# Kernel optimization log

Measured on AMD Instinct MI355X. Metric: run time of the kernel, lower is better.

Reference implementation:

```python
import jax, jax.numpy as jnp
import numpy as np

HIDDEN = 1024
HEADS = 16
BATCH = 2
SEQ = 2048
# dropout_p = 0.1 but module evaluated in eval mode (training=False) -> identity


def setup_inputs() -> dict:
    key = jax.random.key(0)
    k1, k2, k3 = jax.random.split(key, 3)
    x = jax.random.normal(k1, (BATCH, SEQ, HIDDEN), dtype=jnp.float32)
    # unit-scaling Linear: weight ~ N(0,1) (reset_parameters uses nn.init.normal_)
    w_qkv = jax.random.normal(k2, (3 * HIDDEN, HIDDEN), dtype=jnp.float32)
    w_o = jax.random.normal(k3, (HIDDEN, HIDDEN), dtype=jnp.float32)
    return {"x": x, "w_qkv": w_qkv, "w_o": w_o}


def reference(x, w_qkv, w_o):
    b, s, hid = x.shape
    heads = HEADS
    d = hid // heads
    # unit-scaled linear (constraint='to_output_scale'): y = x @ W.T * fan_in**-0.5
    qkv = (x @ w_qkv.T) * (hid ** -0.5)            # [b, s, 3*hid]
    # einops 'b s (z h d) -> z b h s d'
    qkv = qkv.reshape(b, s, 3, heads, d)
    q = jnp.transpose(qkv[:, :, 0], (0, 2, 1, 3))   # [b, h, s, d]
    k = jnp.transpose(qkv[:, :, 1], (0, 2, 1, 3))
    v = jnp.transpose(qkv[:, :, 2], (0, 2, 1, 3))
    # unit-scaled matmul: scale = inner_dim**-0.5
    scores = jnp.einsum('bhqd,bhkd->bhqk', q, k) * (d ** -0.5)  # [b, h, s, s]
    # unit-scaled softmax: output_scale = n / sqrt(n - 1)
    attn = jax.nn.softmax(scores, axis=-1) * (s / np.sqrt(s - 1.0))
    # dropout inactive (eval mode)
    out = jnp.einsum('bhqk,bhkd->bhqd', attn, v) * (s ** -0.5)  # inner dim = s
    out = jnp.transpose(out, (0, 2, 1, 3)).reshape(b, s, hid)   # 'b h s d -> b s (h d)'
    return (out @ w_o.T) * (hid ** -0.5)
```

## Files before the change

kernel.cpp:

```cpp
#include <hip/hip_runtime.h>

typedef unsigned short u16;
typedef _Float16 f16x8 __attribute__((ext_vector_type(8)));
typedef float f32x4 __attribute__((ext_vector_type(4)));
typedef unsigned short u16x4 __attribute__((ext_vector_type(4)));

#define HID 1024
#define SEQ 2048
#define NH 16
#define DH 64

__device__ __forceinline__ u16 f2h(float f) {
  return __builtin_bit_cast(u16, (_Float16)f);
}
__device__ __forceinline__ f32x4 mfma_h(f16x8 a, f16x8 b, f32x4 c) {
  return __builtin_amdgcn_mfma_f32_16x16x32_f16(a, b, c, 0, 0, 0);
}
__device__ __forceinline__ float fexp2(float x) {
#if __has_builtin(__builtin_amdgcn_exp2f)
  return __builtin_amdgcn_exp2f(x);
#else
  return __expf(0.69314718f * x);
#endif
}
__device__ __forceinline__ void g2l16(const u16* g, u16* l) {
  __builtin_amdgcn_global_load_lds(
      (const __attribute__((address_space(1))) unsigned int*)g,
      (__attribute__((address_space(3))) unsigned int*)l, 16, 0, 0);
}

#define NX4 ((4096 * 1024) / 4)
#define NQ4 ((3072 * 1024) / 4)
#define NO4 ((1024 * 1024) / 4)
__global__ __launch_bounds__(256) void prep_kernel(
    const float* __restrict__ x, const float* __restrict__ wq,
    const float* __restrict__ wo,
    u16* __restrict__ x16, u16* __restrict__ wq16,
    u16* __restrict__ wo_h, u16* __restrict__ wo_l) {
  int i = blockIdx.x * 256 + threadIdx.x;
  if (i < NX4) {
    const float4 v = ((const float4*)x)[i];
    u16x4 o;
    o[0] = f2h(v.x); o[1] = f2h(v.y); o[2] = f2h(v.z); o[3] = f2h(v.w);
    *(u16x4*)&x16[i * 4] = o;
  } else if (i < NX4 + NQ4) {
    int k = i - NX4;
    const float4 v = ((const float4*)wq)[k];
    u16x4 o;
    o[0] = f2h(v.x); o[1] = f2h(v.y); o[2] = f2h(v.z); o[3] = f2h(v.w);
    *(u16x4*)&wq16[k * 4] = o;
  } else {
    int k = i - NX4 - NQ4;
    const float4 v = ((const float4*)wo)[k];
    float vv[4] = {v.x, v.y, v.z, v.w};
    u16x4 h, l;
#pragma unroll
    for (int j = 0; j < 4; ++j) {
      _Float16 hh = (_Float16)vv[j];
      h[j] = __builtin_bit_cast(u16, hh);
      l[j] = f2h(vv[j] - (float)hh);
    }
    *(u16x4*)&wo_h[k * 4] = h;
    *(u16x4*)&wo_l[k * 4] = l;
  }
}

__global__ __launch_bounds__(256, 3) void gemm_qkv(
    const u16* __restrict__ a16, const u16* __restrict__ b16,
    u16* __restrict__ qf, u16* __restrict__ kf, u16* __restrict__ vtf) {
  __shared__ __align__(16) u16 la[128 * 32], lb[128 * 32];
  const int t = threadIdx.x;
  const int lane = t & 63, w = t >> 6;
  const int wr = w >> 1, wc = w & 1;
  const int lr = lane & 15, lg = lane >> 4;
  const int br = blockIdx.x, bc = blockIdx.y;
  const f32x4 fzero = {0.f, 0.f, 0.f, 0.f};
  f32x4 acc[4][4];
#pragma unroll
  for (int i = 0; i < 4; ++i)
#pragma unroll
    for (int j = 0; j < 4; ++j) acc[i][j] = fzero;
  const int srow = t >> 2, scol = (t & 3) << 3;
  const u16* ga = a16 + (size_t)(br * 128 + srow) * HID + scol;
  const u16* gb = b16 + (size_t)(bc * 128 + srow) * HID + scol;
  const int lo16 = t * 8;
  for (int kk = 0; kk < HID; kk += 32) {
    g2l16(ga + kk, &la[lo16]);
    g2l16(ga + kk + (size_t)64 * HID, &la[lo16 + 2048]);
    g2l16(gb + kk, &lb[lo16]);
    g2l16(gb + kk + (size_t)64 * HID, &lb[lo16 + 2048]);
    __syncthreads();
    f16x8 ah[4], bh[4];
#pragma unroll
    for (int i = 0; i < 4; ++i)
      ah[i] = *(const f16x8*)&la[(wr * 64 + i * 16 + lr) * 32 + lg * 8];
#pragma unroll
    for (int j = 0; j < 4; ++j)
      bh[j] = *(const f16x8*)&lb[(wc * 64 + j * 16 + lr) * 32 + lg * 8];
#pragma unroll
    for (int i = 0; i < 4; ++i)
#pragma unroll
      for (int j = 0; j < 4; ++j) acc[i][j] = mfma_h(ah[i], bh[j], acc[i][j]);
    __syncthreads();
  }
  const int m0 = br * 128 + wr * 64, n0 = bc * 128 + wc * 64;
#pragma unroll
  for (int i = 0; i < 4; ++i)
#pragma unroll
    for (int j = 0; j < 4; ++j)
#pragma unroll
      for (int r = 0; r < 4; ++r) {
        int row = m0 + i * 16 + lg * 4 + r;
        int col = n0 + j * 16 + lr;
        float val = acc[i][j][r] * 0.03125f;
        int b = row >> 11, s = row & 2047;
        int z = col >> 10, hh = (col >> 6) & 15, d = col & 63;
        int bhid = b * NH + hh;
        if (z == 0) {
          qf[((size_t)bhid * SEQ + s) * DH + d] = f2h(val * 0.18033688f);
        } else if (z == 1) {
          kf[((size_t)bhid * SEQ + s) * DH + d] = f2h(val);
        } else {
          int s2 = (s & ~63) | ((s & 15) << 2) | ((s >> 4) & 3);
          vtf[((size_t)bhid * DH + d) * SEQ + s2] = f2h(val);
        }
      }
}

__global__ __launch_bounds__(256, 2) void gemm_proj(
    const u16* __restrict__ a16,
    const u16* __restrict__ b_hi, const u16* __restrict__ b_lo,
    float* __restrict__ out) {
  __shared__ __align__(16) u16 la[128 * 32];
  __shared__ __align__(16) u16 lbh[64 * 32], lbl[64 * 32];
  const int t = threadIdx.x;
  const int lane = t & 63, w = t >> 6;
  const int wr = w >> 1, wc = w & 1;
  const int lr = lane & 15, lg = lane >> 4;
  const int br = blockIdx.x, bc = blockIdx.y;
  const f32x4 fzero = {0.f, 0.f, 0.f, 0.f};
  f32x4 acc[4][2];
#pragma unroll
  for (int i = 0; i < 4; ++i)
#pragma unroll
    for (int j = 0; j < 2; ++j) acc[i][j] = fzero;
  const int srow = t >> 2, scol = (t & 3) << 3;
  const u16* ga = a16 + (size_t)(br * 128 + srow) * HID + scol;
  const u16* gbh = b_hi + (size_t)(bc * 64 + srow) * HID + scol;
  const u16* gbl = b_lo + (size_t)(bc * 64 + srow) * HID + scol;
  const int lo16 = t * 8;
  for (int kk = 0; kk < HID; kk += 32) {
    g2l16(ga + kk, &la[lo16]);
    g2l16(ga + kk + (size_t)64 * HID, &la[lo16 + 2048]);
    g2l16(gbh + kk, &lbh[lo16]);
    g2l16(gbl + kk, &lbl[lo16]);
    __syncthreads();
    f16x8 ah[4], bh[2], bl[2];
#pragma unroll
    for (int i = 0; i < 4; ++i)
      ah[i] = *(const f16x8*)&la[(wr * 64 + i * 16 + lr) * 32 + lg * 8];
#pragma unroll
    for (int j = 0; j < 2; ++j) {
      int o = (wc * 32 + j * 16 + lr) * 32 + lg * 8;
      bh[j] = *(const f16x8*)&lbh[o];
      bl[j] = *(const f16x8*)&lbl[o];
    }
#pragma unroll
    for (int i = 0; i < 4; ++i)
#pragma unroll
      for (int j = 0; j < 2; ++j) {
        acc[i][j] = mfma_h(ah[i], bh[j], acc[i][j]);
        acc[i][j] = mfma_h(ah[i], bl[j], acc[i][j]);
      }
    __syncthreads();
  }
  const int m0 = br * 128 + wr * 64, n0 = bc * 64 + wc * 32;
#pragma unroll
  for (int i = 0; i < 4; ++i)
#pragma unroll
    for (int j = 0; j < 2; ++j)
#pragma unroll
      for (int r = 0; r < 4; ++r) {
        int row = m0 + i * 16 + lg * 4 + r;
        int col = n0 + j * 16 + lr;
        out[(size_t)row * HID + col] = acc[i][j][r] * 0.03125f;
      }
}

__global__ __launch_bounds__(256, 2) void attn_kernel(
    const u16* __restrict__ qf, const u16* __restrict__ kf,
    const u16* __restrict__ vtf, u16* __restrict__ o16) {
  __shared__ __align__(16) u16 lk[2][64 * 64];
  __shared__ __align__(16) u16 lv[2][64 * 64];
  __shared__ __align__(16) u16 lp[128 * 64];
  const int t = threadIdx.x;
  const int lane = t & 63, w = t >> 6;
  const int lr = lane & 15, lg = lane >> 4;
  const int bh = blockIdx.x, qt = blockIdx.y;
  const size_t base_qk = (size_t)bh * SEQ * DH;
  const size_t base_vt = (size_t)bh * DH * SEQ;

  f16x8 qfr[2][2];
#pragma unroll
  for (int rt = 0; rt < 2; ++rt)
#pragma unroll
    for (int ks = 0; ks < 2; ++ks)
      qfr[rt][ks] = *(const f16x8*)&qf[base_qk +
          (size_t)(qt * 128 + w * 32 + rt * 16 + lr) * DH + ks * 32 + lg * 8];

  const f32x4 fzero = {0.f, 0.f, 0.f, 0.f};
  f32x4 acc_o[2][4];
  float l_i[2][4];
#pragma unroll
  for (int rt = 0; rt < 2; ++rt)
#pragma unroll
    for (int r = 0; r < 4; ++r) l_i[rt][r] = 0.f;
#pragma unroll
  for (int rt = 0; rt < 2; ++rt)
#pragma unroll
    for (int ct = 0; ct < 4; ++ct) acc_o[rt][ct] = fzero;

  const int srow = t >> 3;
  const int scol = ((t & 7) ^ (srow & 7)) << 3;
  const int lo16 = t * 8;

  const u16* gk0 = kf + base_qk + (size_t)srow * DH + scol;
  const u16* gv0 = vtf + base_vt + (size_t)srow * SEQ + scol;

#define STAGE(buf, j)                                             \
  {                                                               \
    const u16* gk = gk0 + (size_t)(j) * 64 * DH;                  \
    g2l16(gk, &lk[buf][lo16]);                                    \
    g2l16(gk + 32 * DH, &lk[buf][lo16 + 2048]);                   \
    const u16* gv = gv0 + (j) * 64;                               \
    g2l16(gv, &lv[buf][lo16]);                                    \
    g2l16(gv + (size_t)32 * SEQ, &lv[buf][lo16 + 2048]);          \
  }

  STAGE(0, 0)

  for (int j = 0; j < SEQ / 64; ++j) {
    const int cur = j & 1;
    __syncthreads();

    f32x4 sa[2][4];
#pragma unroll
    for (int rt = 0; rt < 2; ++rt)
#pragma unroll
      for (int ct = 0; ct < 4; ++ct) sa[rt][ct] = fzero;
#pragma unroll
    for (int ks = 0; ks < 2; ++ks)
#pragma unroll
      for (int ct = 0; ct < 4; ++ct) {
        int row = ct * 16 + lr;
        f16x8 kfr = *(const f16x8*)&lk[cur][row * 64 + (((ks * 4 + lg) ^ (row & 7)) << 3)];
#pragma unroll
        for (int rt = 0; rt < 2; ++rt) sa[rt][ct] = mfma_h(qfr[rt][ks], kfr, sa[rt][ct]);
      }

#pragma unroll
    for (int rt = 0; rt < 2; ++rt)
#pragma unroll
      for (int r = 0; r < 4; ++r) {
        float p0 = fexp2(sa[rt][0][r]);
        float p1 = fexp2(sa[rt][1][r]);
        float p2 = fexp2(sa[rt][2][r]);
        float p3 = fexp2(sa[rt][3][r]);
        l_i[rt][r] += (p0 + p1) + (p2 + p3);
        int prow = w * 32 + rt * 16 + lg * 4 + r;
        u16x4 pk;
        pk[0] = f2h(p0); pk[1] = f2h(p1); pk[2] = f2h(p2); pk[3] = f2h(p3);
        int phys = prow * 64 + ((((lr >> 1) ^ (prow & 7)) << 3) | ((lr & 1) << 2));
        *(u16x4*)&lp[phys] = pk;
      }
    __syncthreads();

    if (j + 1 < SEQ / 64) STAGE(cur ^ 1, j + 1)

#pragma unroll
    for (int ks = 0; ks < 2; ++ks) {
      f16x8 pfr[2];
#pragma unroll
      for (int rt = 0; rt < 2; ++rt) {
        int prow = w * 32 + rt * 16 + lr;
        pfr[rt] = *(const f16x8*)&lp[prow * 64 + (((ks * 4 + lg) ^ (prow & 7)) << 3)];
      }
#pragma unroll
      for (int ct = 0; ct < 4; ++ct) {
        int vrow = ct * 16 + lr;
        f16x8 vfr = *(const f16x8*)&lv[cur][vrow * 64 + (((ks * 4 + lg) ^ (vrow & 7)) << 3)];
#pragma unroll
        for (int rt = 0; rt < 2; ++rt) acc_o[rt][ct] = mfma_h(pfr[rt], vfr, acc_o[rt][ct]);
      }
    }
  }

#pragma unroll
  for (int rt = 0; rt < 2; ++rt)
#pragma unroll
    for (int r = 0; r < 4; ++r) {
      float l = l_i[rt][r];
      l += __shfl_xor(l, 1, 16);
      l += __shfl_xor(l, 2, 16);
      l += __shfl_xor(l, 4, 16);
      l += __shfl_xor(l, 8, 16);
      l_i[rt][r] = l;
    }

  const int b = bh >> 4, hh = bh & 15;
  const float fact = 1.00024426f;
#pragma unroll
  for (int rt = 0; rt < 2; ++rt)
#pragma unroll
    for (int r = 0; r < 4; ++r) {
      float inv = fact / l_i[rt][r];
      int s = qt * 128 + w * 32 + rt * 16 + lg * 4 + r;
#pragma unroll
      for (int ct = 0; ct < 4; ++ct) {
        int d = ct * 16 + lr;
        float val = acc_o[rt][ct][r] * inv;
        o16[((size_t)(b * SEQ + s)) * HID + hh * DH + d] = f2h(val);
      }
    }
}

extern "C" void kernel_launch(void* const* d_in, const int* in_sizes, int n_in,
                              void* d_out, int out_size, void* d_ws, size_t ws_size,
                              hipStream_t stream) {
  const float* x = (const float*)d_in[0];
  const float* w_qkv = (const float*)d_in[1];
  const float* w_o = (const float*)d_in[2];
  u16* ws = (u16*)d_ws;
  const size_t XS = (size_t)4096 * 1024;
  const size_t WQ = (size_t)3072 * 1024;
  const size_t WO = (size_t)1024 * 1024;
  u16* x16  = ws;           u16* wq16 = x16 + XS;
  u16* wo_h = wq16 + WQ;    u16* wo_l = wo_h + WO;
  u16* q_f  = wo_l + WO;    u16* k_f  = q_f + XS;
  u16* vt_f = k_f + XS;     u16* o16  = vt_f + XS;

  prep_kernel<<<(NX4 + NQ4 + NO4) / 256, 256, 0, stream>>>(
      x, w_qkv, w_o, x16, wq16, wo_h, wo_l);
  gemm_qkv<<<dim3(32, 24), 256, 0, stream>>>(x16, wq16, q_f, k_f, vt_f);
  attn_kernel<<<dim3(32, 16), 256, 0, stream>>>(q_f, k_f, vt_f, o16);
  gemm_proj<<<dim3(32, 16), 256, 0, stream>>>(o16, wo_h, wo_l, (float*)d_out);
}
```

Baseline: 189.8 us.

## Drop split-fp16 output weights, use 2-wave attention blocks, pack P conversion

Stops splitting the output-projection weight into hi/lo fp16 halves, which halves the MFMA count and B-tile traffic in gemm_proj at some cost in precision. The attention kernel now uses 128 threads per block, with each wave owning 64 query rows instead of 32. This doubles K/V fragment reuse per LDS read but raises register pressure and halves the waves available per block. The P tile is converted with packed cvt_pkrtz into a single 64-bit store, and the prep kernel is simplified to a single branchless conversion path.

```diff
diff --git a/kernel.cpp b/kernel.cpp
--- a/kernel.cpp
+++ b/kernel.cpp
@@ -23,6 +23,9 @@
   return __expf(0.69314718f * x);
 #endif
 }
+__device__ __forceinline__ unsigned pk2h(float a, float b) {
+  return __builtin_bit_cast(unsigned, __builtin_amdgcn_cvt_pkrtz(a, b));
+}
 __device__ __forceinline__ void g2l16(const u16* g, u16* l) {
   __builtin_amdgcn_global_load_lds(
       (const __attribute__((address_space(1))) unsigned int*)g,
@@ -35,34 +38,17 @@
 __global__ __launch_bounds__(256) void prep_kernel(
     const float* __restrict__ x, const float* __restrict__ wq,
     const float* __restrict__ wo,
-    u16* __restrict__ x16, u16* __restrict__ wq16,
-    u16* __restrict__ wo_h, u16* __restrict__ wo_l) {
+    u16* __restrict__ x16, u16* __restrict__ wq16, u16* __restrict__ wo16) {
   int i = blockIdx.x * 256 + threadIdx.x;
-  if (i < NX4) {
-    const float4 v = ((const float4*)x)[i];
-    u16x4 o;
-    o[0] = f2h(v.x); o[1] = f2h(v.y); o[2] = f2h(v.z); o[3] = f2h(v.w);
-    *(u16x4*)&x16[i * 4] = o;
-  } else if (i < NX4 + NQ4) {
-    int k = i - NX4;
-    const float4 v = ((const float4*)wq)[k];
-    u16x4 o;
-    o[0] = f2h(v.x); o[1] = f2h(v.y); o[2] = f2h(v.z); o[3] = f2h(v.w);
-    *(u16x4*)&wq16[k * 4] = o;
-  } else {
-    int k = i - NX4 - NQ4;
-    const float4 v = ((const float4*)wo)[k];
-    float vv[4] = {v.x, v.y, v.z, v.w};
-    u16x4 h, l;
-#pragma unroll
-    for (int j = 0; j < 4; ++j) {
-      _Float16 hh = (_Float16)vv[j];
-      h[j] = __builtin_bit_cast(u16, hh);
-      l[j] = f2h(vv[j] - (float)hh);
-    }
-    *(u16x4*)&wo_h[k * 4] = h;
-    *(u16x4*)&wo_l[k * 4] = l;
-  }
+  const float4 v = (i < NX4) ? ((const float4*)x)[i]
+                 : (i < NX4 + NQ4) ? ((const float4*)wq)[i - NX4]
+                 : ((const float4*)wo)[i - NX4 - NQ4];
+  u16* dst = (i < NX4) ? &x16[(size_t)i * 4]
+           : (i < NX4 + NQ4) ? &wq16[(size_t)(i - NX4) * 4]
+           : &wo16[(size_t)(i - NX4 - NQ4) * 4];
+  u16x4 o;
+  o[0] = f2h(v.x); o[1] = f2h(v.y); o[2] = f2h(v.z); o[3] = f2h(v.w);
+  *(u16x4*)dst = o;
 }
 
 __global__ __launch_bounds__(256, 3) void gemm_qkv(
@@ -128,11 +114,10 @@
 }
 
 __global__ __launch_bounds__(256, 2) void gemm_proj(
-    const u16* __restrict__ a16,
-    const u16* __restrict__ b_hi, const u16* __restrict__ b_lo,
+    const u16* __restrict__ a16, const u16* __restrict__ b16,
     float* __restrict__ out) {
   __shared__ __align__(16) u16 la[128 * 32];
-  __shared__ __align__(16) u16 lbh[64 * 32], lbl[64 * 32];
+  __shared__ __align__(16) u16 lb[64 * 32];
   const int t = threadIdx.x;
   const int lane = t & 63, w = t >> 6;
   const int wr = w >> 1, wc = w & 1;
@@ -146,32 +131,25 @@
     for (int j = 0; j < 2; ++j) acc[i][j] = fzero;
   const int srow = t >> 2, scol = (t & 3) << 3;
   const u16* ga = a16 + (size_t)(br * 128 + srow) * HID + scol;
-  const u16* gbh = b_hi + (size_t)(bc * 64 + srow) * HID + scol;
-  const u16* gbl = b_lo + (size_t)(bc * 64 + srow) * HID + scol;
+  const u16* gb = b16 + (size_t)(bc * 64 + srow) * HID + scol;
   const int lo16 = t * 8;
   for (int kk = 0; kk < HID; kk += 32) {
     g2l16(ga + kk, &la[lo16]);
     g2l16(ga + kk + (size_t)64 * HID, &la[lo16 + 2048]);
-    g2l16(gbh + kk, &lbh[lo16]);
-    g2l16(gbl + kk, &lbl[lo16]);
-    __syncthreads();
-    f16x8 ah[4], bh[2], bl[2];
+    g2l16(gb + kk, &lb[lo16]);
+    __syncthreads();
+    f16x8 ah[4], bh[2];
 #pragma unroll
     for (int i = 0; i < 4; ++i)
       ah[i] = *(const f16x8*)&la[(wr * 64 + i * 16 + lr) * 32 + lg * 8];
 #pragma unroll
-    for (int j = 0; j < 2; ++j) {
-      int o = (wc * 32 + j * 16 + lr) * 32 + lg * 8;
-      bh[j] = *(const f16x8*)&lbh[o];
-      bl[j] = *(const f16x8*)&lbl[o];
-    }
+    for (int j = 0; j < 2; ++j)
+      bh[j] = *(const f16x8*)&lb[(wc * 32 + j * 16 + lr) * 32 + lg * 8];
 #pragma unroll
     for (int i = 0; i < 4; ++i)
 #pragma unroll
-      for (int j = 0; j < 2; ++j) {
+      for (int j = 0; j < 2; ++j)
         acc[i][j] = mfma_h(ah[i], bh[j], acc[i][j]);
-        acc[i][j] = mfma_h(ah[i], bl[j], acc[i][j]);
-      }
     __syncthreads();
   }
   const int m0 = br * 128 + wr * 64, n0 = bc * 64 + wc * 32;
@@ -187,7 +165,7 @@
       }
 }
 
-__global__ __launch_bounds__(256, 2) void attn_kernel(
+__global__ __launch_bounds__(128, 2) void attn_kernel(
     const u16* __restrict__ qf, const u16* __restrict__ kf,
     const u16* __restrict__ vtf, u16* __restrict__ o16) {
   __shared__ __align__(16) u16 lk[2][64 * 64];
@@ -200,41 +178,45 @@
   const size_t base_qk = (size_t)bh * SEQ * DH;
   const size_t base_vt = (size_t)bh * DH * SEQ;
 
-  f16x8 qfr[2][2];
-#pragma unroll
-  for (int rt = 0; rt < 2; ++rt)
+  f16x8 qfr[4][2];
+#pragma unroll
+  for (int rt = 0; rt < 4; ++rt)
 #pragma unroll
     for (int ks = 0; ks < 2; ++ks)
       qfr[rt][ks] = *(const f16x8*)&qf[base_qk +
-          (size_t)(qt * 128 + w * 32 + rt * 16 + lr) * DH + ks * 32 + lg * 8];
+          (size_t)(qt * 128 + w * 64 + rt * 16 + lr) * DH + ks * 32 + lg * 8];
 
   const f32x4 fzero = {0.f, 0.f, 0.f, 0.f};
-  f32x4 acc_o[2][4];
-  float l_i[2][4];
-#pragma unroll
-  for (int rt = 0; rt < 2; ++rt)
+  f32x4 acc_o[4][4];
+  float l_i[4][4];
+#pragma unroll
+  for (int rt = 0; rt < 4; ++rt)
 #pragma unroll
     for (int r = 0; r < 4; ++r) l_i[rt][r] = 0.f;
 #pragma unroll
-  for (int rt = 0; rt < 2; ++rt)
+  for (int rt = 0; rt < 4; ++rt)
 #pragma unroll
     for (int ct = 0; ct < 4; ++ct) acc_o[rt][ct] = fzero;
 
-  const int srow = t >> 3;
-  const int scol = ((t & 7) ^ (srow & 7)) << 3;
+  const int srow0 = t >> 3;
+  const int scol = ((t & 7) ^ (srow0 & 7)) << 3;
   const int lo16 = t * 8;
 
-  const u16* gk0 = kf + base_qk + (size_t)srow * DH + scol;
-  const u16* gv0 = vtf + base_vt + (size_t)srow * SEQ + scol;
-
-#define STAGE(buf, j)                                             \
-  {                                                               \
-    const u16* gk = gk0 + (size_t)(j) * 64 * DH;                  \
-    g2l16(gk, &lk[buf][lo16]);                                    \
-    g2l16(gk + 32 * DH, &lk[buf][lo16 + 2048]);                   \
-    const u16* gv = gv0 + (j) * 64;                               \
-    g2l16(gv, &lv[buf][lo16]);                                    \
-    g2l16(gv + (size_t)32 * SEQ, &lv[buf][lo16 + 2048]);          \
+  const u16* gk0 = kf + base_qk + (size_t)srow0 * DH + scol;
+  const u16* gv0 = vtf + base_vt + (size_t)srow0 * SEQ + scol;
+
+#define STAGE(buf, j)                                               \
+  {                                                                 \
+    const u16* gk = gk0 + (size_t)(j) * 64 * DH;                    \
+    g2l16(gk, &lk[buf][lo16]);                                      \
+    g2l16(gk + 16 * DH, &lk[buf][lo16 + 1024]);                     \
+    g2l16(gk + 32 * DH, &lk[buf][lo16 + 2048]);                     \
+    g2l16(gk + 48 * DH, &lk[buf][lo16 + 3072]);                     \
+    const u16* gv = gv0 + (j) * 64;                                 \
+    g2l16(gv, &lv[buf][lo16]);                                      \
+    g2l16(gv + (size_t)16 * SEQ, &lv[buf][lo16 + 1024]);            \
+    g2l16(gv + (size_t)32 * SEQ, &lv[buf][lo16 + 2048]);            \
+    g2l16(gv + (size_t)48 * SEQ, &lv[buf][lo16 + 3072]);            \
   }
 
   STAGE(0, 0)
@@ -243,9 +225,9 @@
     const int cur = j & 1;
     __syncthreads();
 
-    f32x4 sa[2][4];
-#pragma unroll
-    for (int rt = 0; rt < 2; ++rt)
+    f32x4 sa[4][4];
+#pragma unroll
+    for (int rt = 0; rt < 4; ++rt)
 #pragma unroll
       for (int ct = 0; ct < 4; ++ct) sa[rt][ct] = fzero;
 #pragma unroll
@@ -255,11 +237,11 @@
         int row = ct * 16 + lr;
         f16x8 kfr = *(const f16x8*)&lk[cur][row * 64 + (((ks * 4 + lg) ^ (row & 7)) << 3)];
 #pragma unroll
-        for (int rt = 0; rt < 2; ++rt) sa[rt][ct] = mfma_h(qfr[rt][ks], kfr, sa[rt][ct]);
-      }
-
-#pragma unroll
-    for (int rt = 0; rt < 2; ++rt)
+        for (int rt = 0; rt < 4; ++rt) sa[rt][ct] = mfma_h(qfr[rt][ks], kfr, sa[rt][ct]);
+      }
+
+#pragma unroll
+    for (int rt = 0; rt < 4; ++rt)
 #pragma unroll
       for (int r = 0; r < 4; ++r) {
         float p0 = fexp2(sa[rt][0][r]);
@@ -267,11 +249,11 @@
         float p2 = fexp2(sa[rt][2][r]);
         float p3 = fexp2(sa[rt][3][r]);
         l_i[rt][r] += (p0 + p1) + (p2 + p3);
-        int prow = w * 32 + rt * 16 + lg * 4 + r;
-        u16x4 pk;
-        pk[0] = f2h(p0); pk[1] = f2h(p1); pk[2] = f2h(p2); pk[3] = f2h(p3);
+        unsigned long long pv = (unsigned long long)pk2h(p0, p1) |
+                                ((unsigned long long)pk2h(p2, p3) << 32);
+        int prow = w * 64 + rt * 16 + lg * 4 + r;
         int phys = prow * 64 + ((((lr >> 1) ^ (prow & 7)) << 3) | ((lr & 1) << 2));
-        *(u16x4*)&lp[phys] = pk;
+        *(unsigned long long*)&lp[phys] = pv;
       }
     __syncthreads();
 
@@ -279,10 +261,10 @@
 
 #pragma unroll
     for (int ks = 0; ks < 2; ++ks) {
-      f16x8 pfr[2];
-#pragma unroll
-      for (int rt = 0; rt < 2; ++rt) {
-        int prow = w * 32 + rt * 16 + lr;
+      f16x8 pfr[4];
+#pragma unroll
+      for (int rt = 0; rt < 4; ++rt) {
+        int prow = w * 64 + rt * 16 + lr;
         pfr[rt] = *(const f16x8*)&lp[prow * 64 + (((ks * 4 + lg) ^ (prow & 7)) << 3)];
       }
 #pragma unroll
@@ -290,13 +272,13 @@
         int vrow = ct * 16 + lr;
         f16x8 vfr = *(const f16x8*)&lv[cur][vrow * 64 + (((ks * 4 + lg) ^ (vrow & 7)) << 3)];
 #pragma unroll
-        for (int rt = 0; rt < 2; ++rt) acc_o[rt][ct] = mfma_h(pfr[rt], vfr, acc_o[rt][ct]);
+        for (int rt = 0; rt < 4; ++rt) acc_o[rt][ct] = mfma_h(pfr[rt], vfr, acc_o[rt][ct]);
       }
     }
   }
 
 #pragma unroll
-  for (int rt = 0; rt < 2; ++rt)
+  for (int rt = 0; rt < 4; ++rt)
 #pragma unroll
     for (int r = 0; r < 4; ++r) {
       float l = l_i[rt][r];
@@ -310,11 +292,11 @@
   const int b = bh >> 4, hh = bh & 15;
   const float fact = 1.00024426f;
 #pragma unroll
-  for (int rt = 0; rt < 2; ++rt)
+  for (int rt = 0; rt < 4; ++rt)
 #pragma unroll
     for (int r = 0; r < 4; ++r) {
       float inv = fact / l_i[rt][r];
-      int s = qt * 128 + w * 32 + rt * 16 + lg * 4 + r;
+      int s = qt * 128 + w * 64 + rt * 16 + lg * 4 + r;
 #pragma unroll
       for (int ct = 0; ct < 4; ++ct) {
         int d = ct * 16 + lr;
@@ -335,13 +317,13 @@
   const size_t WQ = (size_t)3072 * 1024;
   const size_t WO = (size_t)1024 * 1024;
   u16* x16  = ws;           u16* wq16 = x16 + XS;
-  u16* wo_h = wq16 + WQ;    u16* wo_l = wo_h + WO;
-  u16* q_f  = wo_l + WO;    u16* k_f  = q_f + XS;
+  u16* wo16 = wq16 + WQ;
+  u16* q_f  = wo16 + WO;    u16* k_f  = q_f + XS;
   u16* vt_f = k_f + XS;     u16* o16  = vt_f + XS;
 
   prep_kernel<<<(NX4 + NQ4 + NO4) / 256, 256, 0, stream>>>(
-      x, w_qkv, w_o, x16, wq16, wo_h, wo_l);
+      x, w_qkv, w_o, x16, wq16, wo16);
   gemm_qkv<<<dim3(32, 24), 256, 0, stream>>>(x16, wq16, q_f, k_f, vt_f);
-  attn_kernel<<<dim3(32, 16), 256, 0, stream>>>(q_f, k_f, vt_f, o16);
-  gemm_proj<<<dim3(32, 16), 256, 0, stream>>>(o16, wo_h, wo_l, (float*)d_out);
-}
+  attn_kernel<<<dim3(32, 16), 128, 0, stream>>>(q_f, k_f, vt_f, o16);
+  gemm_proj<<<dim3(32, 16), 256, 0, stream>>>(o16, wo16, (float*)d_out);
+}
```

Measured after the change: 205.8 us. +8.4%, slower.
